# Kernel optimization log

Hardware: AMD Instinct MI355X
Metric: run time of the kernel (lower is better)

## Reference

```python
import jax, jax.numpy as jnp
import numpy as np

B, N, C, H = 4096, 49, 128, 4
DH = C // H  # head dim = 32
SCALE = DH ** -0.5

def setup_inputs() -> dict:
    key = jax.random.key(0)
    kx, kq, kp, kb = jax.random.split(key, 4)
    x = jax.random.normal(kx, (B, N, C), dtype=jnp.float32)
    w_qkv = jax.random.normal(kq, (C, 3 * C), dtype=jnp.float32) * (C ** -0.5)
    w_proj = jax.random.normal(kp, (C, C), dtype=jnp.float32) * (C ** -0.5)
    b_proj = jax.random.normal(kb, (C,), dtype=jnp.float32) * 0.01
    return {"x": x, "w_qkv": w_qkv, "w_proj": w_proj, "b_proj": b_proj}

def reference(x, w_qkv, w_proj, b_proj):
    Bx, Nx, Cx = x.shape
    qkv = x @ w_qkv  # (B, N, 3C)
    q, k, v = jnp.split(qkv, 3, axis=-1)
    # (B, N, C) -> (B, H, N, DH)
    def heads(t):
        return t.reshape(Bx, Nx, H, DH).transpose(0, 2, 1, 3)
    q, k, v = heads(q), heads(k), heads(v)
    attn = jnp.einsum('bhnd,bhmd->bhnm', q, k) * SCALE
    attn = jax.nn.softmax(attn, axis=-1)
    out = jnp.einsum('bhnm,bhmd->bhnd', attn, v)
    out = out.transpose(0, 2, 1, 3).reshape(Bx, Nx, Cx)
    return out @ w_proj + b_proj
```

## Files before the change

kernel.cpp:

```cpp
#include <hip/hip_runtime.h>
#include <hip/hip_bf16.h>

typedef unsigned short u16;
typedef unsigned int u32;
typedef __bf16 bf16;
typedef __attribute__((ext_vector_type(8))) __bf16 bf16x8;
typedef __attribute__((ext_vector_type(4))) __bf16 bf16x4;
typedef __attribute__((ext_vector_type(4))) float f32x4;

#define MFMA16(A,B,C) __builtin_amdgcn_mfma_f32_16x16x32_bf16(A,B,C,0,0,0)

constexpr int NTOK = 49;
constexpr int CH   = 128;
constexpr float CEXP = 0.17677669529663687f * 1.4426950408889634f;

__device__ __forceinline__ bf16x8 lds_v8(const char* p) {
    return *reinterpret_cast<const bf16x8*>(p);
}
__device__ __forceinline__ void lds_st64(char* p, float a0, float a1, float a2, float a3) {
    bf16x4 v = {(bf16)a0, (bf16)a1, (bf16)a2, (bf16)a3};
    *reinterpret_cast<bf16x4*>(p) = v;
}
__device__ __forceinline__ u32 pkbf(float a, float b) {
    u16 lo = __builtin_bit_cast(u16, (bf16)a);
    u16 hi = __builtin_bit_cast(u16, (bf16)b);
    return (u32)lo | ((u32)hi << 16);
}

__device__ __forceinline__ bf16x8 xchg(u32 lo0, u32 lo1, u32 hi0, u32 hi1,
                                       int srcA, int srcB, bool hiT) {
    u32 a0 = __shfl(lo0, srcA), b0 = __shfl(hi0, srcA);
    u32 a1 = __shfl(lo1, srcA), b1 = __shfl(hi1, srcA);
    u32 a2 = __shfl(lo0, srcB), b2 = __shfl(hi0, srcB);
    u32 a3 = __shfl(lo1, srcB), b3 = __shfl(hi1, srcB);
    uint4 u = { hiT ? b0 : a0, hiT ? b1 : a1, hiT ? b2 : a2, hiT ? b3 : a3 };
    return __builtin_bit_cast(bf16x8, u);
}

__global__ void prep_weights_kernel(const float* __restrict__ wqkv,
                                    const float* __restrict__ wproj,
                                    bf16* __restrict__ ws) {
    int i = blockIdx.x * 256 + threadIdx.x;
    if (i < 384 * 128) {
        int n = i >> 7, k = i & 127;
        ws[i] = (bf16)wqkv[k * 384 + n];
    }
    if (i < 128 * 128) {
        int n = i >> 7, k = i & 127;
        ws[384 * 128 + i] = (bf16)wproj[k * 128 + n];
    }
}

__launch_bounds__(256, 4)
__global__ void fused_window_attn(const float* __restrict__ x,
                                  const bf16* __restrict__ wqkv_t,
                                  const bf16* __restrict__ wproj_t,
                                  const float* __restrict__ bias,
                                  float* __restrict__ out) {
    __shared__ __align__(16) u16 smem[16384];
    char* S8 = reinterpret_cast<char*>(smem);

    const int tid  = threadIdx.x;
    const int blk  = blockIdx.x;
    const int h    = tid >> 6;
    const int lane = tid & 63;
    const int lr   = lane & 15;
    const int lg   = lane >> 4;
    const int srcA = lr + 32 * (lg & 1);
    const int srcB = srcA + 16;
    const bool hiT = (lg >= 2);

    char* Vb = S8 + 16384 + h * 4096;

    const float* xw = x + (size_t)blk * (NTOK * CH);
    #pragma unroll
    for (int it = 0; it < 7; ++it) {
        int i = tid + it * 256;
        if (i < (NTOK * CH) / 4) {
            float4 v = reinterpret_cast<const float4*>(xw)[i];
            int e = i * 4, row = e >> 7, col = e & 127;
            bf16x4 pk4 = { (bf16)v.x, (bf16)v.y, (bf16)v.z, (bf16)v.w };
            *reinterpret_cast<bf16x4*>(S8 + row * 256 + ((col * 2) ^ ((row & 7) << 4))) = pk4;
        }
    }
    if (tid < 240) {
        uint4 zz = {0, 0, 0, 0};
        *reinterpret_cast<uint4*>(S8 + 49 * 256 + tid * 16) = zz;
    }
    __syncthreads();

    bf16x8 xf[4][4];
    #pragma unroll
    for (int tt = 0; tt < 4; ++tt)
        #pragma unroll
        for (int ks = 0; ks < 4; ++ks) {
            int row = tt * 16 + lr;
            xf[tt][ks] = lds_v8(S8 + row * 256 + ((ks * 64 + lg * 16) ^ ((row & 7) << 4)));
        }

    __builtin_amdgcn_s_setprio(1);
    #pragma unroll
    for (int i = 0; i < 2; ++i) {
        int ct = 16 + 2 * h + i;
        bf16x8 wf[4];
        const bf16* wrow = wqkv_t + (ct * 16 + lr) * 128 + lg * 8;
        #pragma unroll
        for (int ks = 0; ks < 4; ++ks)
            wf[ks] = *reinterpret_cast<const bf16x8*>(wrow + ks * 32);
        int dh = i * 16 + lr;
        #pragma unroll
        for (int tt = 0; tt < 4; ++tt) {
            f32x4 a = {0.f, 0.f, 0.f, 0.f};
            #pragma unroll
            for (int ks = 0; ks < 4; ++ks) a = MFMA16(xf[tt][ks], wf[ks], a);
            lds_st64(Vb + dh * 128 + ((tt * 32 + lg * 8) ^ ((dh & 7) << 4)),
                     a[0], a[1], a[2], a[3]);
        }
    }

    bf16x8 qf[4];
    {
        u32 pkq[2][4][2];
        #pragma unroll
        for (int half = 0; half < 2; ++half) {
            int ct = 2 * h + half;
            bf16x8 wf[4];
            const bf16* wrow = wqkv_t + (ct * 16 + lr) * 128 + lg * 8;
            #pragma unroll
            for (int ks = 0; ks < 4; ++ks)
                wf[ks] = *reinterpret_cast<const bf16x8*>(wrow + ks * 32);
            #pragma unroll
            for (int tt = 0; tt < 4; ++tt) {
                f32x4 a = {0.f, 0.f, 0.f, 0.f};
                #pragma unroll
                for (int ks = 0; ks < 4; ++ks) a = MFMA16(wf[ks], xf[tt][ks], a);
                pkq[half][tt][0] = pkbf(a[0], a[1]);
                pkq[half][tt][1] = pkbf(a[2], a[3]);
            }
        }
        #pragma unroll
        for (int tt = 0; tt < 4; ++tt)
            qf[tt] = xchg(pkq[0][tt][0], pkq[0][tt][1],
                          pkq[1][tt][0], pkq[1][tt][1], srcA, srcB, hiT);
    }
    bf16x8 kf[4];
    {
        u32 pkk[2][4][2];
        #pragma unroll
        for (int half = 0; half < 2; ++half) {
            int ct = 8 + 2 * h + half;
            bf16x8 wf[4];
            const bf16* wrow = wqkv_t + (ct * 16 + lr) * 128 + lg * 8;
            #pragma unroll
            for (int ks = 0; ks < 4; ++ks)
                wf[ks] = *reinterpret_cast<const bf16x8*>(wrow + ks * 32);
            #pragma unroll
            for (int tt = 0; tt < 4; ++tt) {
                f32x4 a = {0.f, 0.f, 0.f, 0.f};
                #pragma unroll
                for (int ks = 0; ks < 4; ++ks) a = MFMA16(wf[ks], xf[tt][ks], a);
                pkk[half][tt][0] = pkbf(a[0], a[1]);
                pkk[half][tt][1] = pkbf(a[2], a[3]);
            }
        }
        #pragma unroll
        for (int tt = 0; tt < 4; ++tt)
            kf[tt] = xchg(pkk[0][tt][0], pkk[0][tt][1],
                          pkk[1][tt][0], pkk[1][tt][1], srcA, srcB, hiT);
    }
    __builtin_amdgcn_s_setprio(0);

    bf16x8 vf[2][2];
    #pragma unroll
    for (int dht = 0; dht < 2; ++dht)
        #pragma unroll
        for (int ks2 = 0; ks2 < 2; ++ks2) {
            int dh = dht * 16 + lr;
            vf[dht][ks2] = lds_v8(Vb + dh * 128 + ((ks2 * 64 + lg * 16) ^ ((dh & 7) << 4)));
        }
    __syncthreads();

    #pragma unroll
    for (int qt = 0; qt < 4; ++qt) {
        f32x4 s[4];
        __builtin_amdgcn_s_setprio(1);
        #pragma unroll
        for (int st = 0; st < 4; ++st) {
            f32x4 z = {0.f, 0.f, 0.f, 0.f};
            s[st] = MFMA16(kf[st], qf[qt], z);
        }
        __builtin_amdgcn_s_setprio(0);
        float l = 0.f;
        #pragma unroll
        for (int st = 0; st < 3; ++st)
            #pragma unroll
            for (int rg = 0; rg < 4; ++rg) {
                float e = exp2f(s[st][rg] * CEXP);
                s[st][rg] = e;
                l += e;
            }
        {
            float e48 = exp2f(s[3][0] * CEXP);
            float v48 = (lg == 0) ? e48 : 0.f;
            s[3][0] = v48; s[3][1] = 0.f; s[3][2] = 0.f; s[3][3] = 0.f;
            l += v48;
        }
        l += __shfl_xor(l, 16);
        l += __shfl_xor(l, 32);
        float rs = 1.f / l;

        u32 pks[4][2];
        #pragma unroll
        for (int st = 0; st < 4; ++st) {
            pks[st][0] = pkbf(s[st][0], s[st][1]);
            pks[st][1] = pkbf(s[st][2], s[st][3]);
        }
        bf16x8 pf0 = xchg(pks[0][0], pks[0][1], pks[1][0], pks[1][1], srcA, srcB, hiT);
        bf16x8 pf1 = xchg(pks[2][0], pks[2][1], pks[3][0], pks[3][1], srcA, srcB, hiT);

        f32x4 o0 = {0.f, 0.f, 0.f, 0.f}, o1 = {0.f, 0.f, 0.f, 0.f};
        __builtin_amdgcn_s_setprio(1);
        o0 = MFMA16(vf[0][0], pf0, o0);
        o1 = MFMA16(vf[1][0], pf0, o1);
        o0 = MFMA16(vf[0][1], pf1, o0);
        o1 = MFMA16(vf[1][1], pf1, o1);
        __builtin_amdgcn_s_setprio(0);

        int q = qt * 16 + lr;
        lds_st64(S8 + q * 256 + ((h * 64 + lg * 8) ^ ((q & 7) << 4)),
                 o0[0] * rs, o0[1] * rs, o0[2] * rs, o0[3] * rs);
        lds_st64(S8 + q * 256 + ((h * 64 + 32 + lg * 8) ^ ((q & 7) << 4)),
                 o1[0] * rs, o1[1] * rs, o1[2] * rs, o1[3] * rs);
    }
    __syncthreads();

    bf16x8 ofr[4][4];
    #pragma unroll
    for (int tt = 0; tt < 4; ++tt)
        #pragma unroll
        for (int ks = 0; ks < 4; ++ks) {
            int row = tt * 16 + lr;
            ofr[tt][ks] = lds_v8(S8 + row * 256 + ((ks * 64 + lg * 16) ^ ((row & 7) << 4)));
        }
    #pragma unroll
    for (int i = 0; i < 2; ++i) {
        int ct = 2 * h + i;
        bf16x8 wf[4];
        const bf16* wrow = wproj_t + (ct * 16 + lr) * 128 + lg * 8;
        #pragma unroll
        for (int ks = 0; ks < 4; ++ks)
            wf[ks] = *reinterpret_cast<const bf16x8*>(wrow + ks * 32);
        float4 bv = *reinterpret_cast<const float4*>(bias + ct * 16 + lg * 4);
        __builtin_amdgcn_s_setprio(1);
        #pragma unroll
        for (int tt = 0; tt < 4; ++tt) {
            f32x4 a = {0.f, 0.f, 0.f, 0.f};
            #pragma unroll
            for (int ks = 0; ks < 4; ++ks) a = MFMA16(wf[ks], ofr[tt][ks], a);
            int tok = tt * 16 + lr;
            if (tok < NTOK) {
                float4 r = { a[0] + bv.x, a[1] + bv.y, a[2] + bv.z, a[3] + bv.w };
                *reinterpret_cast<float4*>(
                    out + ((size_t)blk * NTOK + tok) * CH + ct * 16 + lg * 4) = r;
            }
        }
        __builtin_amdgcn_s_setprio(0);
    }
}

extern "C" void kernel_launch(void* const* d_in, const int* in_sizes, int n_in,
                              void* d_out, int out_size, void* d_ws, size_t ws_size,
                              hipStream_t stream) {
    const float* x     = (const float*)d_in[0];
    const float* wqkv  = (const float*)d_in[1];
    const float* wproj = (const float*)d_in[2];
    const float* bias  = (const float*)d_in[3];
    float* out = (float*)d_out;
    bf16* ws   = (bf16*)d_ws;

    constexpr size_t WS_NEED = (size_t)(384 * 128 + 128 * 128) * sizeof(u16);
    if (ws_size < WS_NEED) return;

    prep_weights_kernel<<<192, 256, 0, stream>>>(wqkv, wproj, ws);
    fused_window_attn<<<4096, 256, 0, stream>>>(x, ws, ws + 384 * 128, bias, out);
}
```

Measured before the change: 91.82 us.

## Split each head across two waves and stage K through LDS

```diff
diff --git a/kernel.cpp b/kernel.cpp
--- a/kernel.cpp
+++ b/kernel.cpp
@@ -51,18 +51,20 @@
     }
 }
 
-__launch_bounds__(256, 4)
+__launch_bounds__(512, 8)
 __global__ void fused_window_attn(const float* __restrict__ x,
                                   const bf16* __restrict__ wqkv_t,
                                   const bf16* __restrict__ wproj_t,
                                   const float* __restrict__ bias,
                                   float* __restrict__ out) {
-    __shared__ __align__(16) u16 smem[16384];
+    __shared__ __align__(16) u16 smem[24576];
     char* S8 = reinterpret_cast<char*>(smem);
 
     const int tid  = threadIdx.x;
     const int blk  = blockIdx.x;
-    const int h    = tid >> 6;
+    const int w    = tid >> 6;
+    const int h    = w >> 1;
+    const int tf   = w & 1;
     const int lane = tid & 63;
     const int lr   = lane & 15;
     const int lg   = lane >> 4;
@@ -70,12 +72,13 @@
     const int srcB = srcA + 16;
     const bool hiT = (lg >= 2);
 
-    char* Vb = S8 + 16384 + h * 4096;
+    char* Kb = S8 + 16384 + h * 4096;
+    char* Vb = S8 + 32768 + h * 4096;
 
     const float* xw = x + (size_t)blk * (NTOK * CH);
     #pragma unroll
-    for (int it = 0; it < 7; ++it) {
-        int i = tid + it * 256;
+    for (int it = 0; it < 4; ++it) {
+        int i = tid + it * 512;
         if (i < (NTOK * CH) / 4) {
             float4 v = reinterpret_cast<const float4*>(xw)[i];
             int e = i * 4, row = e >> 7, col = e & 127;
@@ -89,87 +92,73 @@
     }
     __syncthreads();
 
-    bf16x8 xf[4][4];
-    #pragma unroll
-    for (int tt = 0; tt < 4; ++tt)
+    auto wfrag_ld = [&](const bf16* wt, int ct, bf16x8 wf[4]) {
+        const bf16* wrow = wt + (ct * 16 + lr) * 128 + lg * 8;
+        #pragma unroll
+        for (int ks = 0; ks < 4; ++ks)
+            wf[ks] = *reinterpret_cast<const bf16x8*>(wrow + ks * 32);
+    };
+
+    bf16x8 qf[2];
+    #pragma unroll
+    for (int m = 0; m < 2; ++m) {
+        const int tt = tf * 2 + m;
+        bf16x8 xm[4];
         #pragma unroll
         for (int ks = 0; ks < 4; ++ks) {
             int row = tt * 16 + lr;
-            xf[tt][ks] = lds_v8(S8 + row * 256 + ((ks * 64 + lg * 16) ^ ((row & 7) << 4)));
-        }
-
-    __builtin_amdgcn_s_setprio(1);
-    #pragma unroll
-    for (int i = 0; i < 2; ++i) {
-        int ct = 16 + 2 * h + i;
-        bf16x8 wf[4];
-        const bf16* wrow = wqkv_t + (ct * 16 + lr) * 128 + lg * 8;
-        #pragma unroll
-        for (int ks = 0; ks < 4; ++ks)
-            wf[ks] = *reinterpret_cast<const bf16x8*>(wrow + ks * 32);
-        int dh = i * 16 + lr;
-        #pragma unroll
-        for (int tt = 0; tt < 4; ++tt) {
-            f32x4 a = {0.f, 0.f, 0.f, 0.f};
-            #pragma unroll
-            for (int ks = 0; ks < 4; ++ks) a = MFMA16(xf[tt][ks], wf[ks], a);
+            xm[ks] = lds_v8(S8 + row * 256 + ((ks * 64 + lg * 16) ^ ((row & 7) << 4)));
+        }
+        __builtin_amdgcn_s_setprio(1);
+        u32 pkq[2][2];
+        #pragma unroll
+        for (int half = 0; half < 2; ++half) {
+            bf16x8 wf[4];
+            wfrag_ld(wqkv_t, 2 * h + half, wf);
+            f32x4 a = {0.f, 0.f, 0.f, 0.f};
+            #pragma unroll
+            for (int ks = 0; ks < 4; ++ks) a = MFMA16(wf[ks], xm[ks], a);
+            pkq[half][0] = pkbf(a[0], a[1]);
+            pkq[half][1] = pkbf(a[2], a[3]);
+        }
+        qf[m] = xchg(pkq[0][0], pkq[0][1], pkq[1][0], pkq[1][1], srcA, srcB, hiT);
+        #pragma unroll
+        for (int half = 0; half < 2; ++half) {
+            bf16x8 wf[4];
+            wfrag_ld(wqkv_t, 8 + 2 * h + half, wf);
+            f32x4 a = {0.f, 0.f, 0.f, 0.f};
+            #pragma unroll
+            for (int ks = 0; ks < 4; ++ks) a = MFMA16(wf[ks], xm[ks], a);
+            int tok = tt * 16 + lr;
+            int dh0 = half * 16 + lg * 4;
+            lds_st64(Kb + tok * 64 + ((dh0 * 2) ^ ((tok & 7) << 3)),
+                     a[0], a[1], a[2], a[3]);
+        }
+        #pragma unroll
+        for (int half = 0; half < 2; ++half) {
+            bf16x8 wf[4];
+            wfrag_ld(wqkv_t, 16 + 2 * h + half, wf);
+            f32x4 a = {0.f, 0.f, 0.f, 0.f};
+            #pragma unroll
+            for (int ks = 0; ks < 4; ++ks) a = MFMA16(xm[ks], wf[ks], a);
+            int dh = half * 16 + lr;
             lds_st64(Vb + dh * 128 + ((tt * 32 + lg * 8) ^ ((dh & 7) << 4)),
                      a[0], a[1], a[2], a[3]);
         }
-    }
-
-    bf16x8 qf[4];
-    {
-        u32 pkq[2][4][2];
-        #pragma unroll
-        for (int half = 0; half < 2; ++half) {
-            int ct = 2 * h + half;
-            bf16x8 wf[4];
-            const bf16* wrow = wqkv_t + (ct * 16 + lr) * 128 + lg * 8;
-            #pragma unroll
-            for (int ks = 0; ks < 4; ++ks)
-                wf[ks] = *reinterpret_cast<const bf16x8*>(wrow + ks * 32);
-            #pragma unroll
-            for (int tt = 0; tt < 4; ++tt) {
-                f32x4 a = {0.f, 0.f, 0.f, 0.f};
-                #pragma unroll
-                for (int ks = 0; ks < 4; ++ks) a = MFMA16(wf[ks], xf[tt][ks], a);
-                pkq[half][tt][0] = pkbf(a[0], a[1]);
-                pkq[half][tt][1] = pkbf(a[2], a[3]);
-            }
-        }
-        #pragma unroll
-        for (int tt = 0; tt < 4; ++tt)
-            qf[tt] = xchg(pkq[0][tt][0], pkq[0][tt][1],
-                          pkq[1][tt][0], pkq[1][tt][1], srcA, srcB, hiT);
-    }
+        __builtin_amdgcn_s_setprio(0);
+    }
+    __syncthreads();
+
     bf16x8 kf[4];
-    {
-        u32 pkk[2][4][2];
-        #pragma unroll
-        for (int half = 0; half < 2; ++half) {
-            int ct = 8 + 2 * h + half;
-            bf16x8 wf[4];
-            const bf16* wrow = wqkv_t + (ct * 16 + lr) * 128 + lg * 8;
-            #pragma unroll
-            for (int ks = 0; ks < 4; ++ks)
-                wf[ks] = *reinterpret_cast<const bf16x8*>(wrow + ks * 32);
-            #pragma unroll
-            for (int tt = 0; tt < 4; ++tt) {
-                f32x4 a = {0.f, 0.f, 0.f, 0.f};
-                #pragma unroll
-                for (int ks = 0; ks < 4; ++ks) a = MFMA16(wf[ks], xf[tt][ks], a);
-                pkk[half][tt][0] = pkbf(a[0], a[1]);
-                pkk[half][tt][1] = pkbf(a[2], a[3]);
-            }
-        }
-        #pragma unroll
-        for (int tt = 0; tt < 4; ++tt)
-            kf[tt] = xchg(pkk[0][tt][0], pkk[0][tt][1],
-                          pkk[1][tt][0], pkk[1][tt][1], srcA, srcB, hiT);
-    }
-    __builtin_amdgcn_s_setprio(0);
-
+    #pragma unroll
+    for (int st = 0; st < 4; ++st) {
+        int tok = st * 16 + lr;
+        int o0 = tok * 64 + ((lg * 16) ^ ((tok & 7) << 3));
+        bf16x4 klo = *reinterpret_cast<const bf16x4*>(Kb + o0);
+        bf16x4 khi = *reinterpret_cast<const bf16x4*>(Kb + (o0 ^ 8));
+        bf16x8 k8 = { klo[0],klo[1],klo[2],klo[3], khi[0],khi[1],khi[2],khi[3] };
+        kf[st] = k8;
+    }
     bf16x8 vf[2][2];
     #pragma unroll
     for (int dht = 0; dht < 2; ++dht)
@@ -178,45 +167,53 @@
             int dh = dht * 16 + lr;
             vf[dht][ks2] = lds_v8(Vb + dh * 128 + ((ks2 * 64 + lg * 16) ^ ((dh & 7) << 4)));
         }
-    __syncthreads();
-
-    #pragma unroll
-    for (int qt = 0; qt < 4; ++qt) {
-        f32x4 s[4];
-        __builtin_amdgcn_s_setprio(1);
-        #pragma unroll
-        for (int st = 0; st < 4; ++st) {
-            f32x4 z = {0.f, 0.f, 0.f, 0.f};
-            s[st] = MFMA16(kf[st], qf[qt], z);
-        }
-        __builtin_amdgcn_s_setprio(0);
+
+    #pragma unroll
+    for (int m = 0; m < 2; ++m) {
+        const int qt = tf * 2 + m;
         float l = 0.f;
-        #pragma unroll
-        for (int st = 0; st < 3; ++st)
+        u32 pk01[4], pk23[4];
+        {
+            f32x4 s0, s1;
+            __builtin_amdgcn_s_setprio(1);
+            { f32x4 z = {0,0,0,0}; s0 = MFMA16(kf[0], qf[m], z); }
+            { f32x4 z = {0,0,0,0}; s1 = MFMA16(kf[1], qf[m], z); }
+            __builtin_amdgcn_s_setprio(0);
             #pragma unroll
             for (int rg = 0; rg < 4; ++rg) {
-                float e = exp2f(s[st][rg] * CEXP);
-                s[st][rg] = e;
+                float e0 = exp2f(s0[rg] * CEXP);
+                float e1 = exp2f(s1[rg] * CEXP);
+                s0[rg] = e0; s1[rg] = e1;
+                l += e0 + e1;
+            }
+            pk01[0] = pkbf(s0[0], s0[1]); pk01[1] = pkbf(s0[2], s0[3]);
+            pk01[2] = pkbf(s1[0], s1[1]); pk01[3] = pkbf(s1[2], s1[3]);
+        }
+        {
+            f32x4 s2, s3;
+            __builtin_amdgcn_s_setprio(1);
+            { f32x4 z = {0,0,0,0}; s2 = MFMA16(kf[2], qf[m], z); }
+            { f32x4 z = {0,0,0,0}; s3 = MFMA16(kf[3], qf[m], z); }
+            __builtin_amdgcn_s_setprio(0);
+            #pragma unroll
+            for (int rg = 0; rg < 4; ++rg) {
+                float e = exp2f(s2[rg] * CEXP);
+                s2[rg] = e;
                 l += e;
             }
-        {
-            float e48 = exp2f(s[3][0] * CEXP);
+            float e48 = exp2f(s3[0] * CEXP);
             float v48 = (lg == 0) ? e48 : 0.f;
-            s[3][0] = v48; s[3][1] = 0.f; s[3][2] = 0.f; s[3][3] = 0.f;
+            s3[0] = v48; s3[1] = 0.f; s3[2] = 0.f; s3[3] = 0.f;
             l += v48;
+            pk23[0] = pkbf(s2[0], s2[1]); pk23[1] = pkbf(s2[2], s2[3]);
+            pk23[2] = pkbf(s3[0], s3[1]); pk23[3] = pkbf(s3[2], s3[3]);
         }
         l += __shfl_xor(l, 16);
         l += __shfl_xor(l, 32);
         float rs = 1.f / l;
 
-        u32 pks[4][2];
-        #pragma unroll
-        for (int st = 0; st < 4; ++st) {
-            pks[st][0] = pkbf(s[st][0], s[st][1]);
-            pks[st][1] = pkbf(s[st][2], s[st][3]);
-        }
-        bf16x8 pf0 = xchg(pks[0][0], pks[0][1], pks[1][0], pks[1][1], srcA, srcB, hiT);
-        bf16x8 pf1 = xchg(pks[2][0], pks[2][1], pks[3][0], pks[3][1], srcA, srcB, hiT);
+        bf16x8 pf0 = xchg(pk01[0], pk01[1], pk01[2], pk01[3], srcA, srcB, hiT);
+        bf16x8 pf1 = xchg(pk23[0], pk23[1], pk23[2], pk23[3], srcA, srcB, hiT);
 
         f32x4 o0 = {0.f, 0.f, 0.f, 0.f}, o1 = {0.f, 0.f, 0.f, 0.f};
         __builtin_amdgcn_s_setprio(1);
@@ -234,30 +231,27 @@
     }
     __syncthreads();
 
-    bf16x8 ofr[4][4];
-    #pragma unroll
-    for (int tt = 0; tt < 4; ++tt)
+    bf16x8 ofr[2][4];
+    #pragma unroll
+    for (int m = 0; m < 2; ++m)
         #pragma unroll
         for (int ks = 0; ks < 4; ++ks) {
-            int row = tt * 16 + lr;
-            ofr[tt][ks] = lds_v8(S8 + row * 256 + ((ks * 64 + lg * 16) ^ ((row & 7) << 4)));
+            int row = (tf * 2 + m) * 16 + lr;
+            ofr[m][ks] = lds_v8(S8 + row * 256 + ((ks * 64 + lg * 16) ^ ((row & 7) << 4)));
         }
     #pragma unroll
     for (int i = 0; i < 2; ++i) {
         int ct = 2 * h + i;
         bf16x8 wf[4];
-        const bf16* wrow = wproj_t + (ct * 16 + lr) * 128 + lg * 8;
-        #pragma unroll
-        for (int ks = 0; ks < 4; ++ks)
-            wf[ks] = *reinterpret_cast<const bf16x8*>(wrow + ks * 32);
+        wfrag_ld(wproj_t, ct, wf);
         float4 bv = *reinterpret_cast<const float4*>(bias + ct * 16 + lg * 4);
         __builtin_amdgcn_s_setprio(1);
         #pragma unroll
-        for (int tt = 0; tt < 4; ++tt) {
-            f32x4 a = {0.f, 0.f, 0.f, 0.f};
-            #pragma unroll
-            for (int ks = 0; ks < 4; ++ks) a = MFMA16(wf[ks], ofr[tt][ks], a);
-            int tok = tt * 16 + lr;
+        for (int m = 0; m < 2; ++m) {
+            f32x4 a = {0.f, 0.f, 0.f, 0.f};
+            #pragma unroll
+            for (int ks = 0; ks < 4; ++ks) a = MFMA16(wf[ks], ofr[m][ks], a);
+            int tok = (tf * 2 + m) * 16 + lr;
             if (tok < NTOK) {
                 float4 r = { a[0] + bv.x, a[1] + bv.y, a[2] + bv.z, a[3] + bv.w };
                 *reinterpret_cast<float4*>(
@@ -282,5 +276,5 @@
     if (ws_size < WS_NEED) return;
 
     prep_weights_kernel<<<192, 256, 0, stream>>>(wqkv, wproj, ws);
-    fused_window_attn<<<4096, 256, 0, stream>>>(x, ws, ws + 384 * 128, bias, out);
-}
+    fused_window_attn<<<4096, 512, 0, stream>>>(x, ws, ws + 384 * 128, bias, out);
+}
```

Measured after the change: 234.7 us. 2.56x slower.

## Stream x tiles from LDS per token tile and raise occupancy to 5 blocks

Applied to the files above, without the earlier changes.

```diff
diff --git a/kernel.cpp b/kernel.cpp
--- a/kernel.cpp
+++ b/kernel.cpp
@@ -51,7 +51,7 @@
     }
 }
 
-__launch_bounds__(256, 4)
+__launch_bounds__(256, 5)
 __global__ void fused_window_attn(const float* __restrict__ x,
                                   const bf16* __restrict__ wqkv_t,
                                   const bf16* __restrict__ wproj_t,
@@ -89,86 +89,95 @@
     }
     __syncthreads();
 
-    bf16x8 xf[4][4];
-    #pragma unroll
-    for (int tt = 0; tt < 4; ++tt)
-        #pragma unroll
-        for (int ks = 0; ks < 4; ++ks) {
-            int row = tt * 16 + lr;
-            xf[tt][ks] = lds_v8(S8 + row * 256 + ((ks * 64 + lg * 16) ^ ((row & 7) << 4)));
-        }
-
-    __builtin_amdgcn_s_setprio(1);
-    #pragma unroll
-    for (int i = 0; i < 2; ++i) {
-        int ct = 16 + 2 * h + i;
-        bf16x8 wf[4];
-        const bf16* wrow = wqkv_t + (ct * 16 + lr) * 128 + lg * 8;
+    auto xm_ld = [&](int tt, bf16x8 xm[4]) {
+        int row = tt * 16 + lr;
+        const char* base = S8 + row * 256;
+        int xr = (row & 7) << 4;
         #pragma unroll
         for (int ks = 0; ks < 4; ++ks)
-            wf[ks] = *reinterpret_cast<const bf16x8*>(wrow + ks * 32);
-        int dh = i * 16 + lr;
-        #pragma unroll
-        for (int tt = 0; tt < 4; ++tt) {
-            f32x4 a = {0.f, 0.f, 0.f, 0.f};
-            #pragma unroll
-            for (int ks = 0; ks < 4; ++ks) a = MFMA16(xf[tt][ks], wf[ks], a);
-            lds_st64(Vb + dh * 128 + ((tt * 32 + lg * 8) ^ ((dh & 7) << 4)),
-                     a[0], a[1], a[2], a[3]);
-        }
+            xm[ks] = lds_v8(base + ((ks * 64 + lg * 16) ^ xr));
+    };
+    auto wf2_ld = [&](const bf16* wt, int ct0, int ct1, bf16x8 wf[2][4]) {
+        #pragma unroll
+        for (int half = 0; half < 2; ++half) {
+            const bf16* wrow = wt + ((half ? ct1 : ct0) * 16 + lr) * 128 + lg * 8;
+            #pragma unroll
+            for (int ks = 0; ks < 4; ++ks)
+                wf[half][ks] = *reinterpret_cast<const bf16x8*>(wrow + ks * 32);
+        }
+    };
+
+    {
+        bf16x8 wf[2][4];
+        wf2_ld(wqkv_t, 16 + 2 * h, 16 + 2 * h + 1, wf);
+        __builtin_amdgcn_s_setprio(1);
+        #pragma unroll
+        for (int tt = 0; tt < 4; ++tt) {
+            bf16x8 xm[4];
+            xm_ld(tt, xm);
+            #pragma unroll
+            for (int i = 0; i < 2; ++i) {
+                f32x4 a = {0.f, 0.f, 0.f, 0.f};
+                #pragma unroll
+                for (int ks = 0; ks < 4; ++ks) a = MFMA16(xm[ks], wf[i][ks], a);
+                int dh = i * 16 + lr;
+                lds_st64(Vb + dh * 128 + ((tt * 32 + lg * 8) ^ ((dh & 7) << 4)),
+                         a[0], a[1], a[2], a[3]);
+            }
+        }
+        __builtin_amdgcn_s_setprio(0);
     }
 
     bf16x8 qf[4];
     {
-        u32 pkq[2][4][2];
-        #pragma unroll
-        for (int half = 0; half < 2; ++half) {
-            int ct = 2 * h + half;
-            bf16x8 wf[4];
-            const bf16* wrow = wqkv_t + (ct * 16 + lr) * 128 + lg * 8;
-            #pragma unroll
-            for (int ks = 0; ks < 4; ++ks)
-                wf[ks] = *reinterpret_cast<const bf16x8*>(wrow + ks * 32);
-            #pragma unroll
-            for (int tt = 0; tt < 4; ++tt) {
-                f32x4 a = {0.f, 0.f, 0.f, 0.f};
-                #pragma unroll
-                for (int ks = 0; ks < 4; ++ks) a = MFMA16(wf[ks], xf[tt][ks], a);
-                pkq[half][tt][0] = pkbf(a[0], a[1]);
-                pkq[half][tt][1] = pkbf(a[2], a[3]);
-            }
-        }
+        bf16x8 wf[2][4];
+        wf2_ld(wqkv_t, 2 * h, 2 * h + 1, wf);
+        u32 pkq[4][2][2];
+        __builtin_amdgcn_s_setprio(1);
+        #pragma unroll
+        for (int tt = 0; tt < 4; ++tt) {
+            bf16x8 xm[4];
+            xm_ld(tt, xm);
+            #pragma unroll
+            for (int half = 0; half < 2; ++half) {
+                f32x4 a = {0.f, 0.f, 0.f, 0.f};
+                #pragma unroll
+                for (int ks = 0; ks < 4; ++ks) a = MFMA16(wf[half][ks], xm[ks], a);
+                pkq[tt][half][0] = pkbf(a[0], a[1]);
+                pkq[tt][half][1] = pkbf(a[2], a[3]);
+            }
+        }
+        __builtin_amdgcn_s_setprio(0);
         #pragma unroll
         for (int tt = 0; tt < 4; ++tt)
-            qf[tt] = xchg(pkq[0][tt][0], pkq[0][tt][1],
-                          pkq[1][tt][0], pkq[1][tt][1], srcA, srcB, hiT);
+            qf[tt] = xchg(pkq[tt][0][0], pkq[tt][0][1],
+                          pkq[tt][1][0], pkq[tt][1][1], srcA, srcB, hiT);
     }
     bf16x8 kf[4];
     {
-        u32 pkk[2][4][2];
-        #pragma unroll
-        for (int half = 0; half < 2; ++half) {
-            int ct = 8 + 2 * h + half;
-            bf16x8 wf[4];
-            const bf16* wrow = wqkv_t + (ct * 16 + lr) * 128 + lg * 8;
-            #pragma unroll
-            for (int ks = 0; ks < 4; ++ks)
-                wf[ks] = *reinterpret_cast<const bf16x8*>(wrow + ks * 32);
-            #pragma unroll
-            for (int tt = 0; tt < 4; ++tt) {
-                f32x4 a = {0.f, 0.f, 0.f, 0.f};
-                #pragma unroll
-                for (int ks = 0; ks < 4; ++ks) a = MFMA16(wf[ks], xf[tt][ks], a);
-                pkk[half][tt][0] = pkbf(a[0], a[1]);
-                pkk[half][tt][1] = pkbf(a[2], a[3]);
-            }
-        }
+        bf16x8 wf[2][4];
+        wf2_ld(wqkv_t, 8 + 2 * h, 8 + 2 * h + 1, wf);
+        u32 pkk[4][2][2];
+        __builtin_amdgcn_s_setprio(1);
+        #pragma unroll
+        for (int tt = 0; tt < 4; ++tt) {
+            bf16x8 xm[4];
+            xm_ld(tt, xm);
+            #pragma unroll
+            for (int half = 0; half < 2; ++half) {
+                f32x4 a = {0.f, 0.f, 0.f, 0.f};
+                #pragma unroll
+                for (int ks = 0; ks < 4; ++ks) a = MFMA16(wf[half][ks], xm[ks], a);
+                pkk[tt][half][0] = pkbf(a[0], a[1]);
+                pkk[tt][half][1] = pkbf(a[2], a[3]);
+            }
+        }
+        __builtin_amdgcn_s_setprio(0);
         #pragma unroll
         for (int tt = 0; tt < 4; ++tt)
-            kf[tt] = xchg(pkk[0][tt][0], pkk[0][tt][1],
-                          pkk[1][tt][0], pkk[1][tt][1], srcA, srcB, hiT);
-    }
-    __builtin_amdgcn_s_setprio(0);
+            kf[tt] = xchg(pkk[tt][0][0], pkk[tt][0][1],
+                          pkk[tt][1][0], pkk[tt][1][1], srcA, srcB, hiT);
+    }
 
     bf16x8 vf[2][2];
     #pragma unroll
@@ -234,37 +243,31 @@
     }
     __syncthreads();
 
-    bf16x8 ofr[4][4];
-    #pragma unroll
-    for (int tt = 0; tt < 4; ++tt)
-        #pragma unroll
-        for (int ks = 0; ks < 4; ++ks) {
-            int row = tt * 16 + lr;
-            ofr[tt][ks] = lds_v8(S8 + row * 256 + ((ks * 64 + lg * 16) ^ ((row & 7) << 4)));
-        }
-    #pragma unroll
-    for (int i = 0; i < 2; ++i) {
-        int ct = 2 * h + i;
-        bf16x8 wf[4];
-        const bf16* wrow = wproj_t + (ct * 16 + lr) * 128 + lg * 8;
-        #pragma unroll
-        for (int ks = 0; ks < 4; ++ks)
-            wf[ks] = *reinterpret_cast<const bf16x8*>(wrow + ks * 32);
-        float4 bv = *reinterpret_cast<const float4*>(bias + ct * 16 + lg * 4);
-        __builtin_amdgcn_s_setprio(1);
-        #pragma unroll
-        for (int tt = 0; tt < 4; ++tt) {
-            f32x4 a = {0.f, 0.f, 0.f, 0.f};
-            #pragma unroll
-            for (int ks = 0; ks < 4; ++ks) a = MFMA16(wf[ks], ofr[tt][ks], a);
+    {
+        bf16x8 wf[2][4];
+        wf2_ld(wproj_t, 2 * h, 2 * h + 1, wf);
+        float4 bv0 = *reinterpret_cast<const float4*>(bias + (2 * h) * 16 + lg * 4);
+        float4 bv1 = *reinterpret_cast<const float4*>(bias + (2 * h + 1) * 16 + lg * 4);
+        #pragma unroll
+        for (int tt = 0; tt < 4; ++tt) {
+            bf16x8 om[4];
+            xm_ld(tt, om);
             int tok = tt * 16 + lr;
-            if (tok < NTOK) {
-                float4 r = { a[0] + bv.x, a[1] + bv.y, a[2] + bv.z, a[3] + bv.w };
-                *reinterpret_cast<float4*>(
-                    out + ((size_t)blk * NTOK + tok) * CH + ct * 16 + lg * 4) = r;
-            }
-        }
-        __builtin_amdgcn_s_setprio(0);
+            __builtin_amdgcn_s_setprio(1);
+            #pragma unroll
+            for (int i = 0; i < 2; ++i) {
+                f32x4 a = {0.f, 0.f, 0.f, 0.f};
+                #pragma unroll
+                for (int ks = 0; ks < 4; ++ks) a = MFMA16(wf[i][ks], om[ks], a);
+                if (tok < NTOK) {
+                    float4 bv = i ? bv1 : bv0;
+                    float4 r = { a[0] + bv.x, a[1] + bv.y, a[2] + bv.z, a[3] + bv.w };
+                    *reinterpret_cast<float4*>(
+                        out + ((size_t)blk * NTOK + tok) * CH + (2 * h + i) * 16 + lg * 4) = r;
+                }
+            }
+            __builtin_amdgcn_s_setprio(0);
+        }
     }
 }
 
```

Measured after the change: 97.35 us. 1.06x slower.
